# Optimization experiments

Hardware: AMD Instinct MI355X
Metric: run time of the kernel (lower is better)

The kernel has to match this reference:

```python
import jax, jax.numpy as jnp
import numpy as np

NUM_EXPERTS = 128
TOP_K = 4
HIDDEN = 2880
T = 8192


def setup_inputs() -> dict:
    key = jax.random.key(0)
    kx, kw = jax.random.split(key)
    x = jax.random.normal(kx, (T, HIDDEN), dtype=jnp.float32)
    weight = jax.random.normal(kw, (NUM_EXPERTS, HIDDEN), dtype=jnp.float32) * 0.02
    bias = jnp.zeros((NUM_EXPERTS,), dtype=jnp.float32)
    return {"x": x, "weight": weight, "bias": bias}


def reference(x, weight, bias):
    # logits: (T, E) = x @ W^T + b
    logits = jnp.einsum("th,eh->te", x, weight) + bias
    # top-k logits per token (softmax AFTER topk, matching HF semantics)
    top_logits, top_indices = jax.lax.top_k(logits, TOP_K)  # (T, K)
    top_scores = jax.nn.softmax(top_logits, axis=-1)
    # histogram of expert assignments == bincount over flattened indices
    flat = top_indices.reshape(-1)
    num_tokens_per_expert = jax.ops.segment_sum(
        jnp.ones_like(flat, dtype=jnp.float32), flat, num_segments=NUM_EXPERTS
    )
    return top_scores, top_indices, num_tokens_per_expert
```

## Files before the change

### kernel.cpp

```cpp
#include <hip/hip_runtime.h>
#include <math.h>

#define T_TOK 8192
#define HID   2880
#define NE    128
#define TOPK  4
#define NKS   (HID / 32)
#define LROW  40

typedef _Float16 f16x8 __attribute__((ext_vector_type(8)));
typedef float    f32x4 __attribute__((ext_vector_type(4)));

__global__ __launch_bounds__(256) void convert_w(const float* __restrict__ w,
                                                 _Float16* __restrict__ wc) {
  const int c = blockIdx.x * 256 + threadIdx.x;
  if (c >= NE * (HID / 8)) return;
  const int n  = c / (HID / 8);
  const int k8 = c % (HID / 8);
  const float4 v0 = *(const float4*)(w + (size_t)n * HID + k8 * 8);
  const float4 v1 = *(const float4*)(w + (size_t)n * HID + k8 * 8 + 4);
  const float f[8] = {v0.x, v0.y, v0.z, v0.w, v1.x, v1.y, v1.z, v1.w};
  f16x8 h, l;
#pragma unroll
  for (int i = 0; i < 8; ++i) {
    const float s = f[i] * 32.0f;
    const _Float16 hi = (_Float16)s;
    h[i] = hi;
    l[i] = (_Float16)(s - (float)hi);
  }
  const int gs   = k8 >> 2;
  const int oct  = k8 & 3;
  const int j    = n >> 4;
  const int lane = (oct << 4) | (n & 15);
  _Float16* base = wc + ((size_t)(gs * 8 + j) * 2) * 512 + lane * 8;
  *(f16x8*)(base)       = h;
  *(f16x8*)(base + 512) = l;
}

__global__ __launch_bounds__(256, 2) void logits_mfma(const float* __restrict__ x,
                                                      const _Float16* __restrict__ wc,
                                                      float* __restrict__ part,
                                                      int split) {
  __shared__ _Float16 xh[128 * LROW];
  __shared__ _Float16 xl[128 * LROW];

  const int t    = threadIdx.x;
  const int s    = blockIdx.x % split;
  const int tile = blockIdx.x / split;
  const int m0   = tile * 128;

  const int lane = t & 63;
  const int wv   = t >> 6;
  const int wm   = wv >> 1;
  const int wn   = wv & 1;

  const int kbase = NKS / split, krem = NKS % split;
  const int cnt   = kbase + (s < krem ? 1 : 0);
  const int st0   = s * kbase + (s < krem ? s : krem);

  const int srow = t >> 1;
  const int skh  = t & 1;

  f32x4 acc[4][4] = {};

  float4 xr[4];
  {
    const float* xp = x + (size_t)(m0 + srow) * HID + st0 * 32 + skh * 16;
#pragma unroll
    for (int q = 0; q < 4; ++q) xr[q] = *(const float4*)(xp + q * 4);
  }

  for (int st = 0; st < cnt; ++st) {
    const int gs = st0 + st;

    f16x8 bh[4], bl[4];
    const _Float16* bp = wc + ((size_t)gs * 8 + wn * 4) * 2 * 512 + lane * 8;
#pragma unroll
    for (int nj = 0; nj < 4; ++nj) {
      bh[nj] = *(const f16x8*)(bp + (size_t)nj * 1024);
      bl[nj] = *(const f16x8*)(bp + (size_t)nj * 1024 + 512);
    }

    __syncthreads();

    {
      union { float4 v[4]; float f[16]; } u;
      u.v[0] = xr[0]; u.v[1] = xr[1]; u.v[2] = xr[2]; u.v[3] = xr[3];
      f16x8 h0, h1, l0, l1;
#pragma unroll
      for (int i = 0; i < 8; ++i) {
        const float a = u.f[i];
        const _Float16 ha = (_Float16)a;
        h0[i] = ha; l0[i] = (_Float16)(a - (float)ha);
        const float b = u.f[i + 8];
        const _Float16 hb = (_Float16)b;
        h1[i] = hb; l1[i] = (_Float16)(b - (float)hb);
      }
      const int off = srow * LROW + skh * 16;
      *(f16x8*)&xh[off]     = h0;
      *(f16x8*)&xh[off + 8] = h1;
      *(f16x8*)&xl[off]     = l0;
      *(f16x8*)&xl[off + 8] = l1;
    }
    __syncthreads();

    if (st + 1 < cnt) {
      const float* xp = x + (size_t)(m0 + srow) * HID + (gs + 1) * 32 + skh * 16;
#pragma unroll
      for (int q = 0; q < 4; ++q) xr[q] = *(const float4*)(xp + q * 4);
    }

#pragma unroll
    for (int mi = 0; mi < 4; ++mi) {
      const int off = (wm * 64 + mi * 16 + (lane & 15)) * LROW + (lane >> 4) * 8;
      const f16x8 ah = *(const f16x8*)&xh[off];
      const f16x8 al = *(const f16x8*)&xl[off];
#pragma unroll
      for (int nj = 0; nj < 4; ++nj) {
        acc[mi][nj] = __builtin_amdgcn_mfma_f32_16x16x32_f16(ah, bh[nj], acc[mi][nj], 0, 0, 0);
        acc[mi][nj] = __builtin_amdgcn_mfma_f32_16x16x32_f16(al, bh[nj], acc[mi][nj], 0, 0, 0);
        acc[mi][nj] = __builtin_amdgcn_mfma_f32_16x16x32_f16(ah, bl[nj], acc[mi][nj], 0, 0, 0);
      }
    }
  }

  float* pl = part + (size_t)s * T_TOK * NE;
  const int r0 = m0 + wm * 64 + (lane >> 4) * 4;
  const int e0 = wn * 64 + (lane & 15);
#pragma unroll
  for (int mi = 0; mi < 4; ++mi)
#pragma unroll
    for (int nj = 0; nj < 4; ++nj) {
      float* pp = pl + (size_t)(r0 + mi * 16) * NE + e0 + nj * 16;
#pragma unroll
      for (int r = 0; r < 4; ++r) pp[(size_t)r * NE] = acc[mi][nj][r] * 0.03125f;
    }
}

__global__ __launch_bounds__(256) void topk_kernel(const float* __restrict__ part,
                                                   const float* __restrict__ bias,
                                                   float* __restrict__ out,
                                                   int split) {
  const int lane = threadIdx.x & 63;
  const int wave = threadIdx.x >> 6;
  const int tok  = blockIdx.x * 4 + wave;

  float v0 = 0.f, v1 = 0.f;
  for (int s = 0; s < split; ++s) {
    const float* prow = part + (size_t)s * T_TOK * NE + (size_t)tok * NE;
    v0 += prow[lane];
    v1 += prow[lane + 64];
  }
  v0 += bias[lane];
  v1 += bias[lane + 64];
  const int i0 = lane, i1 = lane + 64;

  float topv[TOPK];
  int   topi[TOPK];

#pragma unroll
  for (int r = 0; r < TOPK; ++r) {
    float bv; int bi;
    if (v0 >= v1) { bv = v0; bi = i0; }
    else          { bv = v1; bi = i1; }
#pragma unroll
    for (int off = 32; off > 0; off >>= 1) {
      const float ov = __shfl_xor(bv, off);
      const int   oi = __shfl_xor(bi, off);
      if (ov > bv || (ov == bv && oi < bi)) { bv = ov; bi = oi; }
    }
    topv[r] = bv; topi[r] = bi;
    if (bi == i0) v0 = -INFINITY;
    if (bi == i1) v1 = -INFINITY;
  }

  const float m = topv[0];
  float sum = 0.f;
#pragma unroll
  for (int r = 0; r < TOPK; ++r) sum += expf(topv[r] - m);

  if (lane < TOPK) {
    out[(size_t)tok * TOPK + lane] = expf(topv[lane] - m) / sum;
    out[(size_t)T_TOK * TOPK + (size_t)tok * TOPK + lane] = (float)topi[lane];
  }
}

__global__ __launch_bounds__(256) void count_kernel(const float* __restrict__ idxf,
                                                    float* __restrict__ counts) {
  const int e = blockIdx.x;
  const int t = threadIdx.x;
  const float ef = (float)e;
  int c = 0;
  for (int i = t; i < T_TOK * TOPK; i += 256)
    c += (idxf[i] == ef) ? 1 : 0;
#pragma unroll
  for (int off = 32; off > 0; off >>= 1) c += __shfl_xor(c, off);
  __shared__ int sh[4];
  if ((t & 63) == 0) sh[t >> 6] = c;
  __syncthreads();
  if (t == 0) counts[e] = (float)(sh[0] + sh[1] + sh[2] + sh[3]);
}

extern "C" void kernel_launch(void* const* d_in, const int* in_sizes, int n_in,
                              void* d_out, int out_size, void* d_ws, size_t ws_size,
                              hipStream_t stream) {
  const float* x    = (const float*)d_in[0];
  const float* w    = (const float*)d_in[1];
  const float* bias = (const float*)d_in[2];
  float* out  = (float*)d_out;
  float* part = (float*)d_ws;

  const size_t plane  = (size_t)T_TOK * NE * sizeof(float);
  const size_t wbytes = (size_t)NE * HID * 2 * sizeof(_Float16);

  int split = (int)((ws_size - wbytes) / plane);
  if (split > 8) split = 8;
  if (split < 1) split = 1;

  _Float16* wc = (_Float16*)((char*)d_ws + (size_t)split * plane);

  convert_w<<<(NE * (HID / 8) + 255) / 256, 256, 0, stream>>>(w, wc);
  logits_mfma<<<(T_TOK / 128) * split, 256, 0, stream>>>(x, wc, part, split);
  topk_kernel<<<T_TOK / 4, 256, 0, stream>>>(part, bias, out, split);
  count_kernel<<<NE, 256, 0, stream>>>(out + (size_t)T_TOK * TOPK,
                                       out + 2 * (size_t)T_TOK * TOPK);
}
```

Baseline: 65.59 us.

## Double-buffer LDS staging in logits GEMM and fold expert counting into top-k

The MFMA logits kernel now uses two LDS buffers and register-prefetched B fragments and x rows two steps ahead. This removes one barrier per K-step and overlaps global loads and fp16 split conversion with the MFMA work. Separately, the count kernel is dropped: counts are zeroed in convert_w and accumulated with float atomicAdd inside topk_kernel, which saves a launch and a rescan of the indices. LDS use doubles, which may affect occupancy, and atomics on 128 addresses add contention.

New measurement: 126.1 us. +92.3%, slower.

```diff
diff --git a/kernel.cpp b/kernel.cpp
--- a/kernel.cpp
+++ b/kernel.cpp
@@ -7,12 +7,15 @@
 #define TOPK  4
 #define NKS   (HID / 32)
 #define LROW  40
+#define LPLANE (128 * LROW)
 
 typedef _Float16 f16x8 __attribute__((ext_vector_type(8)));
 typedef float    f32x4 __attribute__((ext_vector_type(4)));
 
 __global__ __launch_bounds__(256) void convert_w(const float* __restrict__ w,
-                                                 _Float16* __restrict__ wc) {
+                                                 _Float16* __restrict__ wc,
+                                                 float* __restrict__ counts) {
+  if (blockIdx.x == 0 && threadIdx.x < NE) counts[threadIdx.x] = 0.0f;
   const int c = blockIdx.x * 256 + threadIdx.x;
   if (c >= NE * (HID / 8)) return;
   const int n  = c / (HID / 8);
@@ -37,12 +40,66 @@
   *(f16x8*)(base + 512) = l;
 }
 
+__device__ __forceinline__ void load_x(const float* __restrict__ x, int m0,
+                                       int srow, int skh, int gs, float4 (&xr)[4]) {
+  const float* xp = x + (size_t)(m0 + srow) * HID + gs * 32 + skh * 16;
+#pragma unroll
+  for (int q = 0; q < 4; ++q) xr[q] = *(const float4*)(xp + q * 4);
+}
+
+__device__ __forceinline__ void load_b(const _Float16* __restrict__ wc, int wn,
+                                       int lane, int gs, f16x8 (&bh)[4], f16x8 (&bl)[4]) {
+  const _Float16* bp = wc + ((size_t)gs * 8 + wn * 4) * 2 * 512 + lane * 8;
+#pragma unroll
+  for (int nj = 0; nj < 4; ++nj) {
+    bh[nj] = *(const f16x8*)(bp + (size_t)nj * 1024);
+    bl[nj] = *(const f16x8*)(bp + (size_t)nj * 1024 + 512);
+  }
+}
+
+__device__ __forceinline__ void stage_x(const float4 (&xr)[4], _Float16* __restrict__ buf,
+                                        int srow, int skh) {
+  union { float4 v[4]; float f[16]; } u;
+  u.v[0] = xr[0]; u.v[1] = xr[1]; u.v[2] = xr[2]; u.v[3] = xr[3];
+  f16x8 h0, h1, l0, l1;
+#pragma unroll
+  for (int i = 0; i < 8; ++i) {
+    const float a = u.f[i];
+    const _Float16 ha = (_Float16)a;
+    h0[i] = ha; l0[i] = (_Float16)(a - (float)ha);
+    const float b = u.f[i + 8];
+    const _Float16 hb = (_Float16)b;
+    h1[i] = hb; l1[i] = (_Float16)(b - (float)hb);
+  }
+  const int off = srow * LROW + skh * 16;
+  *(f16x8*)&buf[off]              = h0;
+  *(f16x8*)&buf[off + 8]          = h1;
+  *(f16x8*)&buf[LPLANE + off]     = l0;
+  *(f16x8*)&buf[LPLANE + off + 8] = l1;
+}
+
+__device__ __forceinline__ void mfma_step(const _Float16* __restrict__ buf,
+                                          const f16x8 (&bh)[4], const f16x8 (&bl)[4],
+                                          int wm, int lane, f32x4 (&acc)[4][4]) {
+#pragma unroll
+  for (int mi = 0; mi < 4; ++mi) {
+    const int off = (wm * 64 + mi * 16 + (lane & 15)) * LROW + (lane >> 4) * 8;
+    const f16x8 ah = *(const f16x8*)&buf[off];
+    const f16x8 al = *(const f16x8*)&buf[LPLANE + off];
+#pragma unroll
+    for (int nj = 0; nj < 4; ++nj) {
+      acc[mi][nj] = __builtin_amdgcn_mfma_f32_16x16x32_f16(ah, bh[nj], acc[mi][nj], 0, 0, 0);
+      acc[mi][nj] = __builtin_amdgcn_mfma_f32_16x16x32_f16(al, bh[nj], acc[mi][nj], 0, 0, 0);
+      acc[mi][nj] = __builtin_amdgcn_mfma_f32_16x16x32_f16(ah, bl[nj], acc[mi][nj], 0, 0, 0);
+    }
+  }
+}
+
 __global__ __launch_bounds__(256, 2) void logits_mfma(const float* __restrict__ x,
                                                       const _Float16* __restrict__ wc,
                                                       float* __restrict__ part,
                                                       int split) {
-  __shared__ _Float16 xh[128 * LROW];
-  __shared__ _Float16 xl[128 * LROW];
+  __shared__ _Float16 xsh[2 * 2 * LPLANE];
 
   const int t    = threadIdx.x;
   const int s    = blockIdx.x % split;
@@ -61,67 +118,35 @@
   const int srow = t >> 1;
   const int skh  = t & 1;
 
+  _Float16* buf0 = xsh;
+  _Float16* buf1 = xsh + 2 * LPLANE;
+
   f32x4 acc[4][4] = {};
-
-  float4 xr[4];
-  {
-    const float* xp = x + (size_t)(m0 + srow) * HID + st0 * 32 + skh * 16;
-#pragma unroll
-    for (int q = 0; q < 4; ++q) xr[q] = *(const float4*)(xp + q * 4);
-  }
-
-  for (int st = 0; st < cnt; ++st) {
-    const int gs = st0 + st;
-
-    f16x8 bh[4], bl[4];
-    const _Float16* bp = wc + ((size_t)gs * 8 + wn * 4) * 2 * 512 + lane * 8;
-#pragma unroll
-    for (int nj = 0; nj < 4; ++nj) {
-      bh[nj] = *(const f16x8*)(bp + (size_t)nj * 1024);
-      bl[nj] = *(const f16x8*)(bp + (size_t)nj * 1024 + 512);
-    }
-
+  float4 xrA[4], xrB[4];
+  f16x8 bAh[4], bAl[4], bBh[4], bBl[4];
+
+  load_x(x, m0, srow, skh, st0, xrA);
+  load_b(wc, wn, lane, st0, bAh, bAl);
+  stage_x(xrA, buf0, srow, skh);
+  if (cnt > 1) load_x(x, m0, srow, skh, st0 + 1, xrB);
+  __syncthreads();
+
+  int st = 0;
+  for (;;) {
+    if (st + 1 < cnt) load_b(wc, wn, lane, st0 + st + 1, bBh, bBl);
+    if (st + 2 < cnt) load_x(x, m0, srow, skh, st0 + st + 2, xrA);
+    mfma_step(buf0, bAh, bAl, wm, lane, acc);
+    if (st + 1 < cnt) stage_x(xrB, buf1, srow, skh);
     __syncthreads();
-
-    {
-      union { float4 v[4]; float f[16]; } u;
-      u.v[0] = xr[0]; u.v[1] = xr[1]; u.v[2] = xr[2]; u.v[3] = xr[3];
-      f16x8 h0, h1, l0, l1;
-#pragma unroll
-      for (int i = 0; i < 8; ++i) {
-        const float a = u.f[i];
-        const _Float16 ha = (_Float16)a;
-        h0[i] = ha; l0[i] = (_Float16)(a - (float)ha);
-        const float b = u.f[i + 8];
-        const _Float16 hb = (_Float16)b;
-        h1[i] = hb; l1[i] = (_Float16)(b - (float)hb);
-      }
-      const int off = srow * LROW + skh * 16;
-      *(f16x8*)&xh[off]     = h0;
-      *(f16x8*)&xh[off + 8] = h1;
-      *(f16x8*)&xl[off]     = l0;
-      *(f16x8*)&xl[off + 8] = l1;
-    }
+    if (st + 1 >= cnt) break;
+
+    if (st + 2 < cnt) load_b(wc, wn, lane, st0 + st + 2, bAh, bAl);
+    if (st + 3 < cnt) load_x(x, m0, srow, skh, st0 + st + 3, xrB);
+    mfma_step(buf1, bBh, bBl, wm, lane, acc);
+    if (st + 2 < cnt) stage_x(xrA, buf0, srow, skh);
     __syncthreads();
-
-    if (st + 1 < cnt) {
-      const float* xp = x + (size_t)(m0 + srow) * HID + (gs + 1) * 32 + skh * 16;
-#pragma unroll
-      for (int q = 0; q < 4; ++q) xr[q] = *(const float4*)(xp + q * 4);
-    }
-
-#pragma unroll
-    for (int mi = 0; mi < 4; ++mi) {
-      const int off = (wm * 64 + mi * 16 + (lane & 15)) * LROW + (lane >> 4) * 8;
-      const f16x8 ah = *(const f16x8*)&xh[off];
-      const f16x8 al = *(const f16x8*)&xl[off];
-#pragma unroll
-      for (int nj = 0; nj < 4; ++nj) {
-        acc[mi][nj] = __builtin_amdgcn_mfma_f32_16x16x32_f16(ah, bh[nj], acc[mi][nj], 0, 0, 0);
-        acc[mi][nj] = __builtin_amdgcn_mfma_f32_16x16x32_f16(al, bh[nj], acc[mi][nj], 0, 0, 0);
-        acc[mi][nj] = __builtin_amdgcn_mfma_f32_16x16x32_f16(ah, bl[nj], acc[mi][nj], 0, 0, 0);
-      }
-    }
+    st += 2;
+    if (st >= cnt) break;
   }
 
   float* pl = part + (size_t)s * T_TOK * NE;
@@ -182,23 +207,8 @@
   if (lane < TOPK) {
     out[(size_t)tok * TOPK + lane] = expf(topv[lane] - m) / sum;
     out[(size_t)T_TOK * TOPK + (size_t)tok * TOPK + lane] = (float)topi[lane];
-  }
-}
-
-__global__ __launch_bounds__(256) void count_kernel(const float* __restrict__ idxf,
-                                                    float* __restrict__ counts) {
-  const int e = blockIdx.x;
-  const int t = threadIdx.x;
-  const float ef = (float)e;
-  int c = 0;
-  for (int i = t; i < T_TOK * TOPK; i += 256)
-    c += (idxf[i] == ef) ? 1 : 0;
-#pragma unroll
-  for (int off = 32; off > 0; off >>= 1) c += __shfl_xor(c, off);
-  __shared__ int sh[4];
-  if ((t & 63) == 0) sh[t >> 6] = c;
-  __syncthreads();
-  if (t == 0) counts[e] = (float)(sh[0] + sh[1] + sh[2] + sh[3]);
+    atomicAdd(out + 2 * (size_t)T_TOK * TOPK + topi[lane], 1.0f);
+  }
 }
 
 extern "C" void kernel_launch(void* const* d_in, const int* in_sizes, int n_in,
@@ -217,11 +227,10 @@
   if (split > 8) split = 8;
   if (split < 1) split = 1;
 
-  _Float16* wc = (_Float16*)((char*)d_ws + (size_t)split * plane);
-
-  convert_w<<<(NE * (HID / 8) + 255) / 256, 256, 0, stream>>>(w, wc);
+  _Float16* wc    = (_Float16*)((char*)d_ws + (size_t)split * plane);
+  float*    cnts  = out + 2 * (size_t)T_TOK * TOPK;
+
+  convert_w<<<(NE * (HID / 8) + 255) / 256, 256, 0, stream>>>(w, wc, cnts);
   logits_mfma<<<(T_TOK / 128) * split, 256, 0, stream>>>(x, wc, part, split);
   topk_kernel<<<T_TOK / 4, 256, 0, stream>>>(part, bias, out, split);
-  count_kernel<<<NE, 256, 0, stream>>>(out + (size_t)T_TOK * TOPK,
-                                       out + 2 * (size_t)T_TOK * TOPK);
-}
+}
```

## Fuse GEMM with top-k softmax, drop split-K partials, double-buffer 32-row tiles

Applied to the files above, without the earlier changes.

Replaces the split-K logits kernel and separate top-k kernel with one fused kernel. Each 512-thread block computes a full-K 32x128 logits tile, double-buffers the x staging and B-fragment loads, then does bias, top-k and softmax out of LDS. This removes the partial-sum writes and reads to global memory and one launch. In exchange, each block now loads the entire converted weight matrix (reuse is only 32 rows per block), and there is less K parallelism per tile.

Result: slower. 87.29 us (+33.1%).

```diff
diff --git a/kernel.cpp b/kernel.cpp
--- a/kernel.cpp
+++ b/kernel.cpp
@@ -5,10 +5,15 @@
 #define HID   2880
 #define NE    128
 #define TOPK  4
-#define NKS   (HID / 32)
-#define LROW  40
+#define BK    64
+#define NK    (HID / BK)
+#define TM    32
+#define LROW  72
+#define LPLANE (TM * LROW)
+#define LCOL  132
 
 typedef _Float16 f16x8 __attribute__((ext_vector_type(8)));
+typedef _Float16 f16x4 __attribute__((ext_vector_type(4)));
 typedef float    f32x4 __attribute__((ext_vector_type(4)));
 
 __global__ __launch_bounds__(256) void convert_w(const float* __restrict__ w,
@@ -37,151 +42,147 @@
   *(f16x8*)(base + 512) = l;
 }
 
-__global__ __launch_bounds__(256, 2) void logits_mfma(const float* __restrict__ x,
-                                                      const _Float16* __restrict__ wc,
-                                                      float* __restrict__ part,
-                                                      int split) {
-  __shared__ _Float16 xh[128 * LROW];
-  __shared__ _Float16 xl[128 * LROW];
+struct BFrag { f16x8 h[2][2], l[2][2]; };
+
+__device__ __forceinline__ void load_b(const _Float16* __restrict__ wc, int wn,
+                                       int lane, int gs, BFrag& f) {
+#pragma unroll
+  for (int g = 0; g < 2; ++g)
+#pragma unroll
+    for (int kc = 0; kc < 2; ++kc) {
+      const int gs32 = 2 * gs + kc;
+      const _Float16* bp = wc + ((size_t)(gs32 * 8 + wn * 2 + g) * 2) * 512 + lane * 8;
+      f.h[g][kc] = *(const f16x8*)bp;
+      f.l[g][kc] = *(const f16x8*)(bp + 512);
+    }
+}
+
+__device__ __forceinline__ void stage_x(const float4& v, _Float16* __restrict__ buf,
+                                        int r, int kq) {
+  const float a[4] = {v.x, v.y, v.z, v.w};
+  f16x4 h, l;
+#pragma unroll
+  for (int i = 0; i < 4; ++i) {
+    const _Float16 hi = (_Float16)a[i];
+    h[i] = hi;
+    l[i] = (_Float16)(a[i] - (float)hi);
+  }
+  const int off = r * LROW + kq * 4;
+  *(f16x4*)&buf[off]          = h;
+  *(f16x4*)&buf[LPLANE + off] = l;
+}
+
+__device__ __forceinline__ void mfma_step(const _Float16* __restrict__ buf,
+                                          const BFrag& f, int wm, int lane,
+                                          f32x4 (&acc)[2]) {
+#pragma unroll
+  for (int kc = 0; kc < 2; ++kc) {
+    const int off = (wm * 16 + (lane & 15)) * LROW + kc * 32 + (lane >> 4) * 8;
+    const f16x8 ah = *(const f16x8*)&buf[off];
+    const f16x8 al = *(const f16x8*)&buf[LPLANE + off];
+#pragma unroll
+    for (int g = 0; g < 2; ++g) {
+      acc[g] = __builtin_amdgcn_mfma_f32_16x16x32_f16(ah, f.h[g][kc], acc[g], 0, 0, 0);
+      acc[g] = __builtin_amdgcn_mfma_f32_16x16x32_f16(al, f.h[g][kc], acc[g], 0, 0, 0);
+      acc[g] = __builtin_amdgcn_mfma_f32_16x16x32_f16(ah, f.l[g][kc], acc[g], 0, 0, 0);
+    }
+  }
+}
+
+__global__ __launch_bounds__(512) void logits_fused(const float* __restrict__ x,
+                                                    const _Float16* __restrict__ wc,
+                                                    const float* __restrict__ bias,
+                                                    float* __restrict__ out) {
+  __shared__ union {
+    _Float16 stage[2][2][LPLANE];
+    float    logits[TM * LCOL];
+  } sh;
 
   const int t    = threadIdx.x;
-  const int s    = blockIdx.x % split;
-  const int tile = blockIdx.x / split;
-  const int m0   = tile * 128;
-
   const int lane = t & 63;
   const int wv   = t >> 6;
-  const int wm   = wv >> 1;
-  const int wn   = wv & 1;
-
-  const int kbase = NKS / split, krem = NKS % split;
-  const int cnt   = kbase + (s < krem ? 1 : 0);
-  const int st0   = s * kbase + (s < krem ? s : krem);
-
-  const int srow = t >> 1;
-  const int skh  = t & 1;
-
-  f32x4 acc[4][4] = {};
-
-  float4 xr[4];
-  {
-    const float* xp = x + (size_t)(m0 + srow) * HID + st0 * 32 + skh * 16;
-#pragma unroll
-    for (int q = 0; q < 4; ++q) xr[q] = *(const float4*)(xp + q * 4);
-  }
-
-  for (int st = 0; st < cnt; ++st) {
-    const int gs = st0 + st;
-
-    f16x8 bh[4], bl[4];
-    const _Float16* bp = wc + ((size_t)gs * 8 + wn * 4) * 2 * 512 + lane * 8;
-#pragma unroll
-    for (int nj = 0; nj < 4; ++nj) {
-      bh[nj] = *(const f16x8*)(bp + (size_t)nj * 1024);
-      bl[nj] = *(const f16x8*)(bp + (size_t)nj * 1024 + 512);
-    }
-
+  const int wm   = wv >> 2;
+  const int wn   = wv & 3;
+  const int m0   = blockIdx.x * TM;
+  const int r    = t >> 4;
+  const int kq   = t & 15;
+
+  const float* xrow = x + (size_t)(m0 + r) * HID + kq * 4;
+
+  f32x4 acc[2] = {};
+  float4 xrA, xrB;
+  BFrag bA, bB;
+
+  xrA = *(const float4*)(xrow);
+  load_b(wc, wn, lane, 0, bA);
+  stage_x(xrA, &sh.stage[0][0][0], r, kq);
+  xrB = *(const float4*)(xrow + BK);
+  __syncthreads();
+
+  int st = 0;
+  for (;;) {
+    if (st + 1 < NK) load_b(wc, wn, lane, st + 1, bB);
+    if (st + 2 < NK) xrA = *(const float4*)(xrow + (st + 2) * BK);
+    mfma_step(&sh.stage[0][0][0], bA, wm, lane, acc);
+    if (st + 1 < NK) stage_x(xrB, &sh.stage[1][0][0], r, kq);
     __syncthreads();
-
-    {
-      union { float4 v[4]; float f[16]; } u;
-      u.v[0] = xr[0]; u.v[1] = xr[1]; u.v[2] = xr[2]; u.v[3] = xr[3];
-      f16x8 h0, h1, l0, l1;
-#pragma unroll
-      for (int i = 0; i < 8; ++i) {
-        const float a = u.f[i];
-        const _Float16 ha = (_Float16)a;
-        h0[i] = ha; l0[i] = (_Float16)(a - (float)ha);
-        const float b = u.f[i + 8];
-        const _Float16 hb = (_Float16)b;
-        h1[i] = hb; l1[i] = (_Float16)(b - (float)hb);
+    if (st + 1 >= NK) break;
+
+    if (st + 2 < NK) load_b(wc, wn, lane, st + 2, bA);
+    if (st + 3 < NK) xrB = *(const float4*)(xrow + (st + 3) * BK);
+    mfma_step(&sh.stage[1][0][0], bB, wm, lane, acc);
+    if (st + 2 < NK) stage_x(xrA, &sh.stage[0][0][0], r, kq);
+    __syncthreads();
+    st += 2;
+    if (st >= NK) break;
+  }
+
+  const int row0 = wm * 16 + (lane >> 4) * 4;
+  const int col0 = wn * 32 + (lane & 15);
+#pragma unroll
+  for (int g = 0; g < 2; ++g) {
+    const float bv = bias[col0 + g * 16];
+#pragma unroll
+    for (int rr = 0; rr < 4; ++rr)
+      sh.logits[(row0 + rr) * LCOL + col0 + g * 16] = acc[g][rr] * 0.03125f + bv;
+  }
+  __syncthreads();
+
+#pragma unroll
+  for (int i = 0; i < 4; ++i) {
+    const int tk = wv * 4 + i;
+    float v0 = sh.logits[tk * LCOL + lane];
+    float v1 = sh.logits[tk * LCOL + 64 + lane];
+    const int i0 = lane, i1 = lane + 64;
+
+    float topv[TOPK];
+    int   topi[TOPK];
+#pragma unroll
+    for (int rr = 0; rr < TOPK; ++rr) {
+      float bv; int bi;
+      if (v0 >= v1) { bv = v0; bi = i0; }
+      else          { bv = v1; bi = i1; }
+#pragma unroll
+      for (int off = 32; off > 0; off >>= 1) {
+        const float ov = __shfl_xor(bv, off);
+        const int   oi = __shfl_xor(bi, off);
+        if (ov > bv || (ov == bv && oi < bi)) { bv = ov; bi = oi; }
       }
-      const int off = srow * LROW + skh * 16;
-      *(f16x8*)&xh[off]     = h0;
-      *(f16x8*)&xh[off + 8] = h1;
-      *(f16x8*)&xl[off]     = l0;
-      *(f16x8*)&xl[off + 8] = l1;
-    }
-    __syncthreads();
-
-    if (st + 1 < cnt) {
-      const float* xp = x + (size_t)(m0 + srow) * HID + (gs + 1) * 32 + skh * 16;
-#pragma unroll
-      for (int q = 0; q < 4; ++q) xr[q] = *(const float4*)(xp + q * 4);
-    }
-
-#pragma unroll
-    for (int mi = 0; mi < 4; ++mi) {
-      const int off = (wm * 64 + mi * 16 + (lane & 15)) * LROW + (lane >> 4) * 8;
-      const f16x8 ah = *(const f16x8*)&xh[off];
-      const f16x8 al = *(const f16x8*)&xl[off];
-#pragma unroll
-      for (int nj = 0; nj < 4; ++nj) {
-        acc[mi][nj] = __builtin_amdgcn_mfma_f32_16x16x32_f16(ah, bh[nj], acc[mi][nj], 0, 0, 0);
-        acc[mi][nj] = __builtin_amdgcn_mfma_f32_16x16x32_f16(al, bh[nj], acc[mi][nj], 0, 0, 0);
-        acc[mi][nj] = __builtin_amdgcn_mfma_f32_16x16x32_f16(ah, bl[nj], acc[mi][nj], 0, 0, 0);
-      }
-    }
-  }
-
-  float* pl = part + (size_t)s * T_TOK * NE;
-  const int r0 = m0 + wm * 64 + (lane >> 4) * 4;
-  const int e0 = wn * 64 + (lane & 15);
-#pragma unroll
-  for (int mi = 0; mi < 4; ++mi)
-#pragma unroll
-    for (int nj = 0; nj < 4; ++nj) {
-      float* pp = pl + (size_t)(r0 + mi * 16) * NE + e0 + nj * 16;
-#pragma unroll
-      for (int r = 0; r < 4; ++r) pp[(size_t)r * NE] = acc[mi][nj][r] * 0.03125f;
-    }
-}
-
-__global__ __launch_bounds__(256) void topk_kernel(const float* __restrict__ part,
-                                                   const float* __restrict__ bias,
-                                                   float* __restrict__ out,
-                                                   int split) {
-  const int lane = threadIdx.x & 63;
-  const int wave = threadIdx.x >> 6;
-  const int tok  = blockIdx.x * 4 + wave;
-
-  float v0 = 0.f, v1 = 0.f;
-  for (int s = 0; s < split; ++s) {
-    const float* prow = part + (size_t)s * T_TOK * NE + (size_t)tok * NE;
-    v0 += prow[lane];
-    v1 += prow[lane + 64];
-  }
-  v0 += bias[lane];
-  v1 += bias[lane + 64];
-  const int i0 = lane, i1 = lane + 64;
-
-  float topv[TOPK];
-  int   topi[TOPK];
-
-#pragma unroll
-  for (int r = 0; r < TOPK; ++r) {
-    float bv; int bi;
-    if (v0 >= v1) { bv = v0; bi = i0; }
-    else          { bv = v1; bi = i1; }
-#pragma unroll
-    for (int off = 32; off > 0; off >>= 1) {
-      const float ov = __shfl_xor(bv, off);
-      const int   oi = __shfl_xor(bi, off);
-      if (ov > bv || (ov == bv && oi < bi)) { bv = ov; bi = oi; }
-    }
-    topv[r] = bv; topi[r] = bi;
-    if (bi == i0) v0 = -INFINITY;
-    if (bi == i1) v1 = -INFINITY;
-  }
-
-  const float m = topv[0];
-  float sum = 0.f;
-#pragma unroll
-  for (int r = 0; r < TOPK; ++r) sum += expf(topv[r] - m);
-
-  if (lane < TOPK) {
-    out[(size_t)tok * TOPK + lane] = expf(topv[lane] - m) / sum;
-    out[(size_t)T_TOK * TOPK + (size_t)tok * TOPK + lane] = (float)topi[lane];
+      topv[rr] = bv; topi[rr] = bi;
+      if (bi == i0) v0 = -INFINITY;
+      if (bi == i1) v1 = -INFINITY;
+    }
+
+    const float m = topv[0];
+    float sum = 0.f;
+#pragma unroll
+    for (int rr = 0; rr < TOPK; ++rr) sum += expf(topv[rr] - m);
+
+    if (lane < TOPK) {
+      const int tok = m0 + tk;
+      out[(size_t)tok * TOPK + lane] = expf(topv[lane] - m) / sum;
+      out[(size_t)T_TOK * TOPK + (size_t)tok * TOPK + lane] = (float)topi[lane];
+    }
   }
 }
 
@@ -195,10 +196,10 @@
     c += (idxf[i] == ef) ? 1 : 0;
 #pragma unroll
   for (int off = 32; off > 0; off >>= 1) c += __shfl_xor(c, off);
-  __shared__ int sh[4];
-  if ((t & 63) == 0) sh[t >> 6] = c;
+  __shared__ int shred[4];
+  if ((t & 63) == 0) shred[t >> 6] = c;
   __syncthreads();
-  if (t == 0) counts[e] = (float)(sh[0] + sh[1] + sh[2] + sh[3]);
+  if (t == 0) counts[e] = (float)(shred[0] + shred[1] + shred[2] + shred[3]);
 }
 
 extern "C" void kernel_launch(void* const* d_in, const int* in_sizes, int n_in,
@@ -207,21 +208,11 @@
   const float* x    = (const float*)d_in[0];
   const float* w    = (const float*)d_in[1];
   const float* bias = (const float*)d_in[2];
-  float* out  = (float*)d_out;
-  float* part = (float*)d_ws;
-
-  const size_t plane  = (size_t)T_TOK * NE * sizeof(float);
-  const size_t wbytes = (size_t)NE * HID * 2 * sizeof(_Float16);
-
-  int split = (int)((ws_size - wbytes) / plane);
-  if (split > 8) split = 8;
-  if (split < 1) split = 1;
-
-  _Float16* wc = (_Float16*)((char*)d_ws + (size_t)split * plane);
+  float* out = (float*)d_out;
+  _Float16* wc = (_Float16*)d_ws;
 
   convert_w<<<(NE * (HID / 8) + 255) / 256, 256, 0, stream>>>(w, wc);
-  logits_mfma<<<(T_TOK / 128) * split, 256, 0, stream>>>(x, wc, part, split);
-  topk_kernel<<<T_TOK / 4, 256, 0, stream>>>(part, bias, out, split);
+  logits_fused<<<T_TOK / TM, 512, 0, stream>>>(x, wc, bias, out);
   count_kernel<<<NE, 256, 0, stream>>>(out + (size_t)T_TOK * TOPK,
                                        out + 2 * (size_t)T_TOK * TOPK);
 }
```
